# Optimization experiments

Measured on AMD Instinct MI355X. Metric: run time of the kernel, lower is better.

## Reference

```python
import jax, jax.numpy as jnp
import numpy as np

N = 50000          # num nodes
E = 800000         # num directed edges
K = 10             # diffusion_iterations
ALPHA = 0.1        # teleportation_probability
D_IN, D_HID, N_CLS = 512, 128, 64


def _gcn_norm(edge_index, n):
    """Add self-loops and compute symmetric GCN normalization (PyG gcn_norm)."""
    loop = jnp.arange(n, dtype=edge_index.dtype)
    src = jnp.concatenate([edge_index[0], loop])  # message sources (x_j)
    dst = jnp.concatenate([edge_index[1], loop])  # aggregation targets
    deg = jax.ops.segment_sum(jnp.ones(src.shape[0], dtype=jnp.float32), dst,
                              num_segments=n)
    dinv = jnp.where(deg > 0, jax.lax.rsqrt(jnp.maximum(deg, 1.0)), 0.0)
    norm = dinv[src] * dinv[dst]  # [E+N]
    return src, dst, norm


def _appnp(x, src, dst, norm, n, k, alpha):
    """x_{t+1} = (1-alpha) * A_hat x_t + alpha * x_0, iterated k times."""
    h0 = x
    def step(xc, _):
        agg = jax.ops.segment_sum(xc[src] * norm[:, None], dst, num_segments=n)
        return (1.0 - alpha) * agg + alpha * h0, None
    xk, _ = jax.lax.scan(step, x, None, length=k)
    return xk


def setup_inputs() -> dict:
    key = jax.random.key(0)
    k1, k2, k3, k4 = jax.random.split(key, 4)
    x = jax.random.normal(k1, (N, D_IN), dtype=jnp.float32)
    edge_index = jax.random.randint(k2, (2, E), 0, N, dtype=jnp.int32)
    W1 = jax.random.normal(k3, (D_HID, D_IN), dtype=jnp.float32) / np.sqrt(D_IN)
    b1 = jnp.zeros((D_HID,), dtype=jnp.float32)
    W2 = jax.random.normal(k4, (N_CLS, D_HID), dtype=jnp.float32) / np.sqrt(D_HID)
    b2 = jnp.zeros((N_CLS,), dtype=jnp.float32)
    return {"x": x, "edge_index": edge_index, "W1": W1, "b1": b1,
            "W2": W2, "b2": b2}


def reference(x, edge_index, W1, b1, W2, b2):
    src, dst, norm = _gcn_norm(edge_index, N)
    # layer 0 (not last): linear + relu; since it is the second-to-last layer,
    # the recorded embedding is APPNP applied to its activation (x itself is
    # NOT replaced by the diffusion, matching the original forward).
    h1 = jax.nn.relu(x @ W1.T + b1)                    # [N, D_HID]
    emb1 = _appnp(h1, src, dst, norm, N, K, ALPHA)     # [N, D_HID]
    # last layer: linear only, then APPNP diffusion
    logits = h1 @ W2.T + b2                            # [N, N_CLS]
    out = _appnp(logits, src, dst, norm, N, K, ALPHA)  # [N, N_CLS]
    return (x, emb1, out)
```

## Files before the change

### kernel.cpp

```cpp
#include <hip/hip_runtime.h>

#define NN    50000
#define EE    800000
#define DIN   512
#define DH    128
#define NC    64
#define KITER 10
#define NSB   196
#define XBLK  6250

typedef __attribute__((ext_vector_type(8))) short short8;
typedef __attribute__((ext_vector_type(4))) short short4v;
typedef __attribute__((ext_vector_type(4))) float f32x4;

static __device__ __forceinline__ float bf2f(short u) {
  unsigned int x = ((unsigned int)(unsigned short)u) << 16;
  return __builtin_bit_cast(float, x);
}
static __device__ __forceinline__ short f2bf(float f) {
  unsigned int x = __builtin_bit_cast(unsigned int, f);
  unsigned int lsb = (x >> 16) & 1u;
  x += 0x7fffu + lsb;
  return (short)(x >> 16);
}

__global__ void k_copy_conv(const f32x4* __restrict__ src, f32x4* __restrict__ dst,
                            short4v* __restrict__ xb) {
  int i = blockIdx.x * 256 + threadIdx.x;
  f32x4 s = src[i];
  dst[i] = s;
  short4v o = { f2bf(s.x), f2bf(s.y), f2bf(s.z), f2bf(s.w) };
  xb[i] = o;
}

__global__ void k_copy4(const f32x4* __restrict__ src, f32x4* __restrict__ dst) {
  int i = blockIdx.x * 256 + threadIdx.x;
  dst[i] = src[i];
}

__global__ void k_f2bv(const float* __restrict__ src, short* __restrict__ dst) {
  int j = (blockIdx.x * 256 + threadIdx.x) * 4;
  f32x4 s = *(const f32x4*)(src + j);
  short4v o = { f2bf(s.x), f2bf(s.y), f2bf(s.z), f2bf(s.w) };
  *(short4v*)(dst + j) = o;
}

__global__ void k_count(const int* __restrict__ ei, int* __restrict__ cnt) {
  int e = blockIdx.x * 256 + threadIdx.x;
  if (e < EE) atomicAdd(&cnt[ei[EE + e]], 1);
}

__global__ __launch_bounds__(256) void k_scan1(const int* __restrict__ cnt,
                                               int* __restrict__ rp,
                                               int* __restrict__ bsum,
                                               float* __restrict__ dinv) {
  __shared__ int wsum[4];
  int t = threadIdx.x, lane = t & 63, w = t >> 6;
  int i = blockIdx.x * 256 + t;
  int x = (i < NN) ? cnt[i] : 0;
  if (i < NN) dinv[i] = rsqrtf((float)(x + 1));
  #pragma unroll
  for (int off = 1; off < 64; off <<= 1) {
    int y = __shfl_up(x, off);
    if (lane >= off) x += y;
  }
  if (lane == 63) wsum[w] = x;
  __syncthreads();
  int woff = 0;
  #pragma unroll
  for (int j = 0; j < 4; ++j) if (j < w) woff += wsum[j];
  x += woff;
  if (i < NN) rp[i + 1] = x;
  if (t == 255) bsum[blockIdx.x] = x;
}

__global__ __launch_bounds__(256) void k_scan2(int* __restrict__ bsum) {
  __shared__ int wsum[4];
  int t = threadIdx.x, lane = t & 63, w = t >> 6;
  int orig = (t < NSB) ? bsum[t] : 0;
  int x = orig;
  #pragma unroll
  for (int off = 1; off < 64; off <<= 1) {
    int y = __shfl_up(x, off);
    if (lane >= off) x += y;
  }
  if (lane == 63) wsum[w] = x;
  __syncthreads();
  int woff = 0;
  #pragma unroll
  for (int j = 0; j < 4; ++j) if (j < w) woff += wsum[j];
  x += woff;
  if (t < NSB) bsum[t] = x - orig;
}

__global__ __launch_bounds__(256) void k_scan3(int* __restrict__ rp,
                                               const int* __restrict__ bsum) {
  int i = blockIdx.x * 256 + threadIdx.x;
  if (i == 0) rp[0] = 0;
  if (i < NN) rp[i + 1] += bsum[blockIdx.x];
}

__global__ void k_fill(const int* __restrict__ ei, const int* __restrict__ rp,
                       int* __restrict__ fill, const float* __restrict__ dinv,
                       int* __restrict__ col, float* __restrict__ val) {
  int e = blockIdx.x * 256 + threadIdx.x;
  if (e < EE) {
    int s = ei[e], d = ei[EE + e];
    int pos = atomicAdd(&fill[d], 1);
    int idx = rp[d] + pos;
    col[idx] = s;
    val[idx] = dinv[s] * dinv[d];
  }
}

__global__ __launch_bounds__(256) void k_gemm1(const short* __restrict__ Xb,
                                               const short* __restrict__ W1b,
                                               const float* __restrict__ B1,
                                               short* __restrict__ h1,
                                               float* __restrict__ st0) {
  int w = threadIdx.x >> 6;
  int lane = threadIdx.x & 63;
  int q = lane >> 4, r = lane & 15;
  int m0 = blockIdx.x * 64 + w * 16;

  f32x4 acc[8];
  #pragma unroll
  for (int i = 0; i < 8; ++i) acc[i] = (f32x4){0.f, 0.f, 0.f, 0.f};

  int row_a = m0 + r;
  if (row_a >= NN) row_a = NN - 1;
  const short* xrow = Xb + (size_t)row_a * DIN + q * 8;

  for (int kc = 0; kc < DIN / 32; ++kc) {
    short8 a = *(const short8*)(xrow + kc * 32);
    #pragma unroll
    for (int nt = 0; nt < 8; ++nt) {
      const short* wrow = W1b + (size_t)(nt * 16 + r) * DIN + q * 8 + kc * 32;
      short8 b = *(const short8*)wrow;
      acc[nt] = __builtin_amdgcn_mfma_f32_16x16x32_bf16(a, b, acc[nt], 0, 0, 0);
    }
  }

  #pragma unroll
  for (int nt = 0; nt < 8; ++nt) {
    int n = nt * 16 + r;
    float bias = B1[n];
    #pragma unroll
    for (int reg = 0; reg < 4; ++reg) {
      int row = m0 + q * 4 + reg;
      if (row < NN) {
        float v = acc[nt][reg] + bias;
        v = v > 0.f ? v : 0.f;
        h1[(size_t)row * DH + n] = f2bf(v);
        st0[(size_t)row * DH + n] = v;
      }
    }
  }
}

__global__ __launch_bounds__(256) void k_step(const int* __restrict__ rp,
                                              const int* __restrict__ col,
                                              const float* __restrict__ val,
                                              const float* __restrict__ dinv,
                                              const float* __restrict__ xc,
                                              const short* __restrict__ h0,
                                              float* __restrict__ xn,
                                              const float* __restrict__ vc,
                                              float* __restrict__ vn,
                                              int first) {
  if (blockIdx.x < NSB) {
    int i = blockIdx.x * 256 + threadIdx.x;
    if (i >= NN) return;
    float s = 0.f;
    int e = rp[i], end = rp[i + 1];
    if (first) {
      for (; e + 4 <= end; e += 4) {
        float v0 = val[e], v1 = val[e+1], v2 = val[e+2], v3 = val[e+3];
        s += v0; s += v1; s += v2; s += v3;
      }
      for (; e < end; ++e) s += val[e];
      float di = dinv[i];
      s += di * di;
    } else {
      for (; e + 4 <= end; e += 4) {
        int c0 = col[e], c1 = col[e+1], c2 = col[e+2], c3 = col[e+3];
        float v0 = val[e]*vc[c0], v1 = val[e+1]*vc[c1];
        float v2 = val[e+2]*vc[c2], v3 = val[e+3]*vc[c3];
        s += v0; s += v1; s += v2; s += v3;
      }
      for (; e < end; ++e) s += val[e] * vc[col[e]];
      float di = dinv[i];
      s += di * di * vc[i];
    }
    vn[i] = 0.9f * s + 0.1f;
    return;
  }
  int g = (blockIdx.x - NSB) * 256 + threadIdx.x;
  int node = g >> 5, lane = g & 31;
  int e = rp[node], end = rp[node + 1];
  const f32x4* xcv = (const f32x4*)xc;
  f32x4 xself = xcv[(size_t)node * 32 + lane];
  short4v hv = ((const short4v*)h0)[(size_t)node * 32 + lane];
  float di = dinv[node];
  f32x4 acc = (f32x4){0.f, 0.f, 0.f, 0.f};
  for (; e + 4 <= end; e += 4) {
    int s0 = col[e], s1 = col[e+1], s2 = col[e+2], s3 = col[e+3];
    float w0 = val[e], w1 = val[e+1], w2 = val[e+2], w3 = val[e+3];
    f32x4 x0 = xcv[(size_t)s0 * 32 + lane];
    f32x4 x1 = xcv[(size_t)s1 * 32 + lane];
    f32x4 x2 = xcv[(size_t)s2 * 32 + lane];
    f32x4 x3 = xcv[(size_t)s3 * 32 + lane];
    acc += x0 * w0;
    acc += x1 * w1;
    acc += x2 * w2;
    acc += x3 * w3;
  }
  for (; e < end; ++e) {
    int s = col[e];
    acc += xcv[(size_t)s * 32 + lane] * val[e];
  }
  acc += xself * (di * di);
  f32x4 h = { bf2f(hv.x), bf2f(hv.y), bf2f(hv.z), bf2f(hv.w) };
  ((f32x4*)xn)[(size_t)node * 32 + lane] = acc * 0.9f + h * 0.1f;
}

__global__ __launch_bounds__(256) void k_gemm2(const float* __restrict__ emb,
                                               const float* __restrict__ W2,
                                               const float* __restrict__ B2,
                                               const float* __restrict__ v,
                                               float* __restrict__ out2) {
  __shared__ float sW[NC][DH + 1];
  __shared__ float sb[NC];
  __shared__ float sE[32][DH + 1];
  int t = threadIdx.x;
  for (int i = t; i < NC * DH; i += 256) sW[i / DH][i % DH] = W2[i];
  if (t < NC) sb[t] = B2[t];
  int n0 = blockIdx.x * 32;
  for (int i = t; i < 32 * DH; i += 256) {
    int nl = i / DH, kk = i % DH;
    int node = n0 + nl;
    sE[nl][kk] = (node < NN) ? emb[(size_t)node * DH + kk] : 0.f;
  }
  __syncthreads();
  int nl = t >> 3, cb = t & 7;
  int node = n0 + nl;
  if (node >= NN) return;
  float vn = v[node];
  #pragma unroll
  for (int j = 0; j < 8; ++j) {
    int c = cb + 8 * j;
    float s = 0.f;
    #pragma unroll 4
    for (int k = 0; k < DH; ++k) s += sE[nl][k] * sW[c][k];
    s += vn * sb[c];
    out2[(size_t)node * NC + c] = s;
  }
}

extern "C" void kernel_launch(void* const* d_in, const int* in_sizes, int n_in,
                              void* d_out, int out_size, void* d_ws, size_t ws_size,
                              hipStream_t stream) {
  const float* X  = (const float*)d_in[0];
  const int*   EI = (const int*)d_in[1];
  const float* W1 = (const float*)d_in[2];
  const float* B1 = (const float*)d_in[3];
  const float* W2 = (const float*)d_in[4];
  const float* B2 = (const float*)d_in[5];

  float* out0 = (float*)d_out;
  float* out1 = (float*)d_out + 25600000;
  float* out2 = (float*)d_out + 32000000;

  char* xr = (char*)d_in[0];
  const size_t XB_BYTES = (size_t)NN * DIN * sizeof(short);
  bool use_ws = (d_ws != nullptr) && (ws_size >= XB_BYTES);

  float* bufB = (float*)(xr);
  short* Xb   = use_ws ? (short*)d_ws : (short*)(xr);
  float* bufA = (float*)(xr + 51200000);
  short* h1   = (short*)(xr + 76800000);
  int*   col  = (int*)  (xr + 89600000);
  float* val  = (float*)(xr + 92800000);
  int*   rp   = (int*)  (xr + 96000000);
  int*   cnt  = (int*)  (xr + 96200192);
  int*   fill = (int*)  (xr + 96400192);
  float* dinv = (float*)(xr + 96600192);
  float* va   = (float*)(xr + 96800192);
  float* vb   = (float*)(xr + 97000192);
  short* W1b  = (short*)(xr + 97200192);
  int*   bsum = (int*)  (xr + 97400192);

  if (use_ws) {
    k_copy_conv<<<dim3(25000), dim3(256), 0, stream>>>(
        (const f32x4*)X, (f32x4*)out0, (short4v*)Xb);
  } else {
    k_copy4<<<dim3(25000), dim3(256), 0, stream>>>((const f32x4*)X, (f32x4*)out0);
    k_f2bv <<<dim3(25000), dim3(256), 0, stream>>>(out0, Xb);
  }
  k_f2bv <<<dim3(64), dim3(256), 0, stream>>>(W1, W1b);

  hipMemsetAsync(cnt, 0, 400000, stream);
  k_count<<<dim3(3125), dim3(256), 0, stream>>>(EI, cnt);
  k_scan1<<<dim3(NSB), dim3(256), 0, stream>>>(cnt, rp, bsum, dinv);
  k_scan2<<<dim3(1),   dim3(256), 0, stream>>>(bsum);
  k_scan3<<<dim3(NSB), dim3(256), 0, stream>>>(rp, bsum);
  k_fill <<<dim3(3125), dim3(256), 0, stream>>>(EI, rp, fill, dinv, col, val);

  k_gemm1<<<dim3(782), dim3(256), 0, stream>>>(Xb, W1b, B1, h1, bufA);

  for (int it = 0; it < KITER; ++it) {
    const float* xc = (it & 1) ? bufB : bufA;
    float*       xn = (it == KITER - 1) ? out1 : ((it & 1) ? bufA : bufB);
    const float* vcp = (it & 1) ? vb : va;
    float*       vnp = (it & 1) ? va : vb;
    k_step<<<dim3(NSB + XBLK), dim3(256), 0, stream>>>(
        rp, col, val, dinv, xc, h1, xn, vcp, vnp, it == 0 ? 1 : 0);
  }

  k_gemm2<<<dim3(1563), dim3(256), 0, stream>>>(out1, W2, B2, va, out2);
}
```

Measured before the change: 1.093 ms.

## Split SpMM feature columns into slices across blocks for cache locality

The diffusion step kernel now gives each block 64 nodes times a 16-float feature slice (4 threads per node) instead of one full 128-float row per 32 threads. Slices are interleaved by block index so that concurrently running blocks read the same narrow column band of the gathered feature matrix. This is meant to shrink the working set of random gathers and improve L2/MALL hit rates. In exchange, the CSR row pointers, column indices and weights are read once per slice (eight times in total), and each gather moves only 64 bytes per node.

```diff
diff --git a/kernel.cpp b/kernel.cpp
--- a/kernel.cpp
+++ b/kernel.cpp
@@ -7,7 +7,7 @@
 #define NC    64
 #define KITER 10
 #define NSB   196
-#define XBLK  6250
+#define XSLB  6256
 
 typedef __attribute__((ext_vector_type(8))) short short8;
 typedef __attribute__((ext_vector_type(4))) short short4v;
@@ -168,8 +168,8 @@
                                               const float* __restrict__ vc,
                                               float* __restrict__ vn,
                                               int first) {
-  if (blockIdx.x < NSB) {
-    int i = blockIdx.x * 256 + threadIdx.x;
+  if (blockIdx.x >= XSLB) {
+    int i = (blockIdx.x - XSLB) * 256 + threadIdx.x;
     if (i >= NN) return;
     float s = 0.f;
     int e = rp[i], end = rp[i + 1];
@@ -195,33 +195,34 @@
     vn[i] = 0.9f * s + 0.1f;
     return;
   }
-  int g = (blockIdx.x - NSB) * 256 + threadIdx.x;
-  int node = g >> 5, lane = g & 31;
+  int s  = blockIdx.x & 7;
+  int c  = blockIdx.x >> 3;
+  int node = c * 64 + (threadIdx.x >> 2);
+  if (node >= NN) return;
+  int fo = s * 16 + (threadIdx.x & 3) * 4;
   int e = rp[node], end = rp[node + 1];
-  const f32x4* xcv = (const f32x4*)xc;
-  f32x4 xself = xcv[(size_t)node * 32 + lane];
-  short4v hv = ((const short4v*)h0)[(size_t)node * 32 + lane];
+  f32x4 xself = *(const f32x4*)(xc + (size_t)node * DH + fo);
+  short4v hv  = *(const short4v*)(h0 + (size_t)node * DH + fo);
   float di = dinv[node];
   f32x4 acc = (f32x4){0.f, 0.f, 0.f, 0.f};
   for (; e + 4 <= end; e += 4) {
     int s0 = col[e], s1 = col[e+1], s2 = col[e+2], s3 = col[e+3];
     float w0 = val[e], w1 = val[e+1], w2 = val[e+2], w3 = val[e+3];
-    f32x4 x0 = xcv[(size_t)s0 * 32 + lane];
-    f32x4 x1 = xcv[(size_t)s1 * 32 + lane];
-    f32x4 x2 = xcv[(size_t)s2 * 32 + lane];
-    f32x4 x3 = xcv[(size_t)s3 * 32 + lane];
+    f32x4 x0 = *(const f32x4*)(xc + (size_t)s0 * DH + fo);
+    f32x4 x1 = *(const f32x4*)(xc + (size_t)s1 * DH + fo);
+    f32x4 x2 = *(const f32x4*)(xc + (size_t)s2 * DH + fo);
+    f32x4 x3 = *(const f32x4*)(xc + (size_t)s3 * DH + fo);
     acc += x0 * w0;
     acc += x1 * w1;
     acc += x2 * w2;
     acc += x3 * w3;
   }
   for (; e < end; ++e) {
-    int s = col[e];
-    acc += xcv[(size_t)s * 32 + lane] * val[e];
+    acc += *(const f32x4*)(xc + (size_t)col[e] * DH + fo) * val[e];
   }
   acc += xself * (di * di);
   f32x4 h = { bf2f(hv.x), bf2f(hv.y), bf2f(hv.z), bf2f(hv.w) };
-  ((f32x4*)xn)[(size_t)node * 32 + lane] = acc * 0.9f + h * 0.1f;
+  *(f32x4*)(xn + (size_t)node * DH + fo) = acc * 0.9f + h * 0.1f;
 }
 
 __global__ __launch_bounds__(256) void k_gemm2(const float* __restrict__ emb,
@@ -313,7 +314,7 @@
     float*       xn = (it == KITER - 1) ? out1 : ((it & 1) ? bufA : bufB);
     const float* vcp = (it & 1) ? vb : va;
     float*       vnp = (it & 1) ? va : vb;
-    k_step<<<dim3(NSB + XBLK), dim3(256), 0, stream>>>(
+    k_step<<<dim3(XSLB + NSB), dim3(256), 0, stream>>>(
         rp, col, val, dinv, xc, h1, xn, vcp, vnp, it == 0 ? 1 : 0);
   }
 
```

Result: slower. 1.577 ms (+44.4%).
